# Performance work log

Hardware: AMD Instinct MI355X
Metric: run time of the kernel (lower is better)

## Reference

```python
import jax, jax.numpy as jnp
import numpy as np

TEMPERATURE = 0.07
ALPHA = 1.0
GAMMA = 2.0
EPS = 1e-12  # F.normalize eps


def _l2_normalize(x):
    # matches F.normalize: x / max(||x||_2, eps)
    norm = jnp.sqrt(jnp.sum(x * x, axis=-1, keepdims=True))
    return x / jnp.maximum(norm, EPS)


def setup_inputs() -> dict:
    key = jax.random.key(0)
    k1, k2 = jax.random.split(key)
    B, D = 8192, 64
    image_features = jax.random.normal(k1, (B, D), dtype=jnp.float32)
    text_features = jax.random.normal(k2, (B, D), dtype=jnp.float32)
    return {"image_features": image_features, "text_features": text_features}


def reference(image_features, text_features):
    img = _l2_normalize(image_features)
    txt = _l2_normalize(text_features)
    logits = jnp.einsum("bd,cd->bc", img, txt) / TEMPERATURE  # [B, B]
    B = logits.shape[0]
    idx = jnp.arange(B)

    logp_row = jax.nn.log_softmax(logits, axis=-1)  # i2t CE source
    logp_col = jax.nn.log_softmax(logits, axis=0)   # t2i CE source

    diag_logp_row = logp_row[idx, idx]
    diag_logp_col = logp_col[idx, idx]

    # focal weight uses ROW-softmax positive prob for BOTH directions (as in source)
    p_pos = jnp.exp(diag_logp_row)
    w = ALPHA * (1.0 - p_pos) ** GAMMA

    focal_i2t = jnp.mean(w * (-diag_logp_row))
    focal_t2i = jnp.mean(w * (-diag_logp_col))
    return (focal_i2t + focal_t2i) / 2.0
```

## Files before the change

kernel.cpp:

```cpp
#include <hip/hip_runtime.h>
#include <hip/hip_bf16.h>


#define NB 8192
#define ND 64

constexpr float INV_T = 1.0f / 0.07f;
constexpr float LOG2E = 1.4426950408889634f;
constexpr float LN2   = 0.6931471805599453f;
constexpr float K1    = INV_T * LOG2E;

typedef float  floatx4 __attribute__((ext_vector_type(4)));
typedef short  bf16x8  __attribute__((ext_vector_type(8)));

__global__ __launch_bounds__(256)
void norm_kernel(const float* __restrict__ img, const float* __restrict__ txt,
                 __hip_bfloat16* __restrict__ imgB,
                 __hip_bfloat16* __restrict__ txtB,
                 float* __restrict__ diag,
                 float* __restrict__ out)
{
    if (blockIdx.x == 0 && threadIdx.x == 0) out[0] = 0.f;
    const int lane = threadIdx.x & 63;
    const int row  = blockIdx.x * 4 + (threadIdx.x >> 6);
    const float x = img[row * ND + lane];
    const float t = txt[row * ND + lane];
    float sx = x * x, st = t * t, sxt = x * t;
    #pragma unroll
    for (int o = 1; o < 64; o <<= 1) {
        sx  += __shfl_xor(sx,  o, 64);
        st  += __shfl_xor(st,  o, 64);
        sxt += __shfl_xor(sxt, o, 64);
    }
    const float nx_den = fmaxf(sqrtf(sx), 1e-12f);
    const float nt_den = fmaxf(sqrtf(st), 1e-12f);
    imgB[row * ND + lane] = __float2bfloat16(x / nx_den * K1);
    txtB[row * ND + lane] = __float2bfloat16(t / nt_den);
    if (lane == 0) diag[row] = sxt / (nx_den * nt_den) * INV_T;
}

__global__ __launch_bounds__(256)
void score_kernel(const __hip_bfloat16* __restrict__ imgB,
                  const __hip_bfloat16* __restrict__ txtB,
                  float* __restrict__ rowPart,
                  float* __restrict__ colPart)
{
    const int wid   = threadIdx.x >> 6;
    const int lane  = threadIdx.x & 63;
    const int gw    = blockIdx.x * 4 + wid;
    const int strip = gw >> 5;
    const int chunk = gw & 31;
    const int m = lane & 15;
    const int q = lane >> 4;

    const bf16x8* __restrict__ A  = (const bf16x8*)imgB;
    const bf16x8* __restrict__ Bp = (const bf16x8*)txtB;

    const int rowbase = strip * 64;
    bf16x8 a[4][2];
    #pragma unroll
    for (int it = 0; it < 4; ++it) {
        const int r = rowbase + it * 16 + m;
        a[it][0] = A[r * 8 + q];
        a[it][1] = A[r * 8 + 4 + q];
    }

    const int colbase = chunk * 256 + m;
    bf16x8 b0 = Bp[colbase * 8 + q];
    bf16x8 b1 = Bp[colbase * 8 + 4 + q];

    float rs[16];
    #pragma unroll
    for (int i = 0; i < 16; ++i) rs[i] = 0.f;

    const floatx4 NEGK = {-K1, -K1, -K1, -K1};

    #pragma unroll 2
    for (int t = 0; t < 16; ++t) {
        const int nn = colbase + (((t + 1) & 15) << 4);
        const bf16x8 pb0 = Bp[nn * 8 + q];
        const bf16x8 pb1 = Bp[nn * 8 + 4 + q];

        float csp[4];
        #pragma unroll
        for (int it = 0; it < 4; ++it) {
            floatx4 z   = __builtin_amdgcn_mfma_f32_16x16x32_bf16(a[it][0], b0, NEGK, 0, 0, 0);
            floatx4 acc = __builtin_amdgcn_mfma_f32_16x16x32_bf16(a[it][1], b1, z,    0, 0, 0);
            const float e0 = __builtin_amdgcn_exp2f(acc[0]);
            const float e1 = __builtin_amdgcn_exp2f(acc[1]);
            const float e2 = __builtin_amdgcn_exp2f(acc[2]);
            const float e3 = __builtin_amdgcn_exp2f(acc[3]);
            rs[it * 4 + 0] += e0;
            rs[it * 4 + 1] += e1;
            rs[it * 4 + 2] += e2;
            rs[it * 4 + 3] += e3;
            csp[it] = (e0 + e1) + (e2 + e3);
        }
        float cs = (csp[0] + csp[1]) + (csp[2] + csp[3]);
        cs += __shfl_xor(cs, 16, 64);
        cs += __shfl_xor(cs, 32, 64);
        if (q == 0) colPart[strip * NB + colbase + (t << 4)] = cs;
        b0 = pb0; b1 = pb1;
    }

    #pragma unroll
    for (int idx = 0; idx < 16; ++idx) {
        float v = rs[idx];
        v += __shfl_xor(v, 1, 64);
        v += __shfl_xor(v, 2, 64);
        v += __shfl_xor(v, 4, 64);
        v += __shfl_xor(v, 8, 64);
        if (m == idx) {
            const int it = idx >> 2, r = idx & 3;
            rowPart[chunk * NB + rowbase + it * 16 + q * 4 + r] = v;
        }
    }
}

__global__ __launch_bounds__(256)
void finish_kernel(const float* __restrict__ rowPart,
                   const float* __restrict__ colPart,
                   const float* __restrict__ diag,
                   float* __restrict__ out)
{
    const int i = blockIdx.x * 256 + threadIdx.x;
    float rowS = 0.f, colS = 0.f;
    #pragma unroll 4
    for (int c = 0; c < 32; ++c)  rowS += rowPart[c * NB + i];
    #pragma unroll 4
    for (int s = 0; s < 128; ++s) colS += colPart[s * NB + i];
    const float d     = diag[i];
    const float lse_r = INV_T + __builtin_amdgcn_logf(rowS) * LN2;
    const float lse_c = INV_T + __builtin_amdgcn_logf(colS) * LN2;
    const float lpr = d - lse_r;
    const float lpc = d - lse_c;
    const float p   = __builtin_amdgcn_exp2f(lpr * LOG2E);
    const float om  = 1.f - p;
    float contrib = om * om * (-lpr - lpc) * (0.5f / (float)NB);

    #pragma unroll
    for (int o = 1; o < 64; o <<= 1) contrib += __shfl_xor(contrib, o, 64);
    __shared__ float red[4];
    if ((threadIdx.x & 63) == 0) red[threadIdx.x >> 6] = contrib;
    __syncthreads();
    if (threadIdx.x == 0)
        atomicAdd(out, red[0] + red[1] + red[2] + red[3]);
}

extern "C" void kernel_launch(void* const* d_in, const int* in_sizes, int n_in,
                              void* d_out, int out_size, void* d_ws, size_t ws_size,
                              hipStream_t stream)
{
    const float* img = (const float*)d_in[0];
    const float* txt = (const float*)d_in[1];

    char* ws = (char*)d_ws;
    __hip_bfloat16* imgB = (__hip_bfloat16*)(ws);
    __hip_bfloat16* txtB = (__hip_bfloat16*)(ws + (1u << 20));
    float* diag    = (float*)(ws + (2u << 20));
    float* rowPart = (float*)(ws + (2u << 20) + (1u << 16));
    float* colPart = (float*)(ws + (3u << 20) + (1u << 16));

    norm_kernel<<<NB / 4, 256, 0, stream>>>(img, txt, imgB, txtB, diag, (float*)d_out);
    score_kernel<<<1024, 256, 0, stream>>>(imgB, txtB, rowPart, colPart);
    finish_kernel<<<NB / 256, 256, 0, stream>>>(rowPart, colPart, diag, (float*)d_out);
}
```

Before: 98.29 us.

## Fuse finish into score kernel via atomic sums and last-block ticket

```diff
diff --git a/kernel.cpp b/kernel.cpp
--- a/kernel.cpp
+++ b/kernel.cpp
@@ -18,11 +18,18 @@
                  __hip_bfloat16* __restrict__ imgB,
                  __hip_bfloat16* __restrict__ txtB,
                  float* __restrict__ diag,
-                 float* __restrict__ out)
+                 float* __restrict__ rowSum,
+                 float* __restrict__ colSum,
+                 unsigned int* __restrict__ counter)
 {
-    if (blockIdx.x == 0 && threadIdx.x == 0) out[0] = 0.f;
-    const int lane = threadIdx.x & 63;
-    const int row  = blockIdx.x * 4 + (threadIdx.x >> 6);
+    const int tid = threadIdx.x;
+    if (blockIdx.x < 32) {
+        rowSum[blockIdx.x * 256 + tid] = 0.f;
+        colSum[blockIdx.x * 256 + tid] = 0.f;
+        if (blockIdx.x == 0 && tid == 0) *counter = 0u;
+    }
+    const int lane = tid & 63;
+    const int row  = blockIdx.x * 4 + (tid >> 6);
     const float x = img[row * ND + lane];
     const float t = txt[row * ND + lane];
     float sx = x * x, st = t * t, sxt = x * t;
@@ -42,11 +49,15 @@
 __global__ __launch_bounds__(256)
 void score_kernel(const __hip_bfloat16* __restrict__ imgB,
                   const __hip_bfloat16* __restrict__ txtB,
-                  float* __restrict__ rowPart,
-                  float* __restrict__ colPart)
+                  const float* __restrict__ diag,
+                  float* __restrict__ rowSum,
+                  float* __restrict__ colSum,
+                  unsigned int* __restrict__ counter,
+                  float* __restrict__ out)
 {
-    const int wid   = threadIdx.x >> 6;
-    const int lane  = threadIdx.x & 63;
+    const int tid  = threadIdx.x;
+    const int wid  = tid >> 6;
+    const int lane = tid & 63;
     const int gw    = blockIdx.x * 4 + wid;
     const int strip = gw >> 5;
     const int chunk = gw & 31;
@@ -99,7 +110,7 @@
         float cs = (csp[0] + csp[1]) + (csp[2] + csp[3]);
         cs += __shfl_xor(cs, 16, 64);
         cs += __shfl_xor(cs, 32, 64);
-        if (q == 0) colPart[strip * NB + colbase + (t << 4)] = cs;
+        if (q == 0) atomicAdd(&colSum[colbase + (t << 4)], cs);
         b0 = pb0; b1 = pb1;
     }
 
@@ -110,41 +121,37 @@
         v += __shfl_xor(v, 2, 64);
         v += __shfl_xor(v, 4, 64);
         v += __shfl_xor(v, 8, 64);
-        if (m == idx) {
-            const int it = idx >> 2, r = idx & 3;
-            rowPart[chunk * NB + rowbase + it * 16 + q * 4 + r] = v;
-        }
+        if (m == idx)
+            atomicAdd(&rowSum[rowbase + ((idx >> 2) << 4) + q * 4 + (idx & 3)], v);
     }
-}
 
-__global__ __launch_bounds__(256)
-void finish_kernel(const float* __restrict__ rowPart,
-                   const float* __restrict__ colPart,
-                   const float* __restrict__ diag,
-                   float* __restrict__ out)
-{
-    const int i = blockIdx.x * 256 + threadIdx.x;
-    float rowS = 0.f, colS = 0.f;
-    #pragma unroll 4
-    for (int c = 0; c < 32; ++c)  rowS += rowPart[c * NB + i];
-    #pragma unroll 4
-    for (int s = 0; s < 128; ++s) colS += colPart[s * NB + i];
-    const float d     = diag[i];
-    const float lse_r = INV_T + __builtin_amdgcn_logf(rowS) * LN2;
-    const float lse_c = INV_T + __builtin_amdgcn_logf(colS) * LN2;
-    const float lpr = d - lse_r;
-    const float lpc = d - lse_c;
-    const float p   = __builtin_amdgcn_exp2f(lpr * LOG2E);
-    const float om  = 1.f - p;
-    float contrib = om * om * (-lpr - lpc) * (0.5f / (float)NB);
+    __shared__ unsigned int s_ticket;
+    __threadfence();
+    __syncthreads();
+    if (tid == 0) s_ticket = atomicAdd(counter, 1u);
+    __syncthreads();
+    if (s_ticket != (unsigned)(gridDim.x - 1)) return;
 
+    float contrib = 0.f;
+    for (int i = tid; i < NB; i += 256) {
+        const float rowS = atomicAdd(&rowSum[i], 0.f);
+        const float colS = atomicAdd(&colSum[i], 0.f);
+        const float d     = diag[i];
+        const float lse_r = INV_T + __builtin_amdgcn_logf(rowS) * LN2;
+        const float lse_c = INV_T + __builtin_amdgcn_logf(colS) * LN2;
+        const float lpr = d - lse_r;
+        const float lpc = d - lse_c;
+        const float p   = __builtin_amdgcn_exp2f(lpr * LOG2E);
+        const float om  = 1.f - p;
+        contrib += om * om * (-lpr - lpc);
+    }
+    contrib *= (0.5f / (float)NB);
     #pragma unroll
     for (int o = 1; o < 64; o <<= 1) contrib += __shfl_xor(contrib, o, 64);
     __shared__ float red[4];
-    if ((threadIdx.x & 63) == 0) red[threadIdx.x >> 6] = contrib;
+    if (lane == 0) red[wid] = contrib;
     __syncthreads();
-    if (threadIdx.x == 0)
-        atomicAdd(out, red[0] + red[1] + red[2] + red[3]);
+    if (tid == 0) out[0] = (red[0] + red[1]) + (red[2] + red[3]);
 }
 
 extern "C" void kernel_launch(void* const* d_in, const int* in_sizes, int n_in,
@@ -157,11 +164,13 @@
     char* ws = (char*)d_ws;
     __hip_bfloat16* imgB = (__hip_bfloat16*)(ws);
     __hip_bfloat16* txtB = (__hip_bfloat16*)(ws + (1u << 20));
-    float* diag    = (float*)(ws + (2u << 20));
-    float* rowPart = (float*)(ws + (2u << 20) + (1u << 16));
-    float* colPart = (float*)(ws + (3u << 20) + (1u << 16));
+    float* diag   = (float*)(ws + (2u << 20));
+    float* rowSum = (float*)(ws + (2u << 20) + (1u << 16));
+    float* colSum = (float*)(ws + (2u << 20) + (2u << 16));
+    unsigned int* counter = (unsigned int*)(ws + (2u << 20) + (3u << 16));
 
-    norm_kernel<<<NB / 4, 256, 0, stream>>>(img, txt, imgB, txtB, diag, (float*)d_out);
-    score_kernel<<<1024, 256, 0, stream>>>(imgB, txtB, rowPart, colPart);
-    finish_kernel<<<NB / 256, 256, 0, stream>>>(rowPart, colPart, diag, (float*)d_out);
+    norm_kernel<<<NB / 4, 256, 0, stream>>>(img, txt, imgB, txtB, diag,
+                                            rowSum, colSum, counter);
+    score_kernel<<<1024, 256, 0, stream>>>(imgB, txtB, diag, rowSum, colSum,
+                                           counter, (float*)d_out);
 }
```

Measured after the change: 153.1 us. +55.8%, slower.
